# Optimization experiments

Hardware: AMD Instinct MI355X
Metric: run time of the kernel (lower is better)

## Reference

```python
import jax, jax.numpy as jnp
import numpy as np

LEAKY_SLOPE = 0.2
DENSITY = 0.05


def setup_inputs() -> dict:
    key = jax.random.key(0)
    k1, k2, k3, k4, k5, k6 = jax.random.split(key, 6)
    N, F_in, F_out = 8192, 128, 64
    h = jax.random.normal(k1, (N, F_in), dtype=jnp.float32)
    # Linear(in, out, bias=False) weight is [out, in]
    W = jax.random.normal(k2, (F_out, F_in), dtype=jnp.float32) * (1.0 / np.sqrt(F_in))
    a_left = jax.random.normal(k3, (F_out,), dtype=jnp.float32) * 0.1
    a_right = jax.random.normal(k4, (F_out,), dtype=jnp.float32) * 0.1
    vals = jax.random.uniform(k5, (N, N), dtype=jnp.float32)
    keep = jax.random.uniform(k6, (N, N)) < DENSITY
    adj = jnp.where(keep, vals, 0.0)  # raw adjacency; self-loops added in reference
    return {"h": h, "W": W, "a_left": a_left, "a_right": a_right, "adj": adj}


def reference(h, W, a_left, a_right, adj):
    N = adj.shape[0]
    A = adj + jnp.eye(N, dtype=adj.dtype)          # A = adjacency + I (self-loops)
    mask = jnp.abs(A) > 0                          # valued-mask support
    Wh = h @ W.T                                   # [N, F_out]
    e_left = Wh @ a_left                           # [N]
    e_right = Wh @ a_right                         # [N]
    e = e_left[:, None] + e_right[None, :]         # [N, N] additive scores
    e = jnp.where(e >= 0, e, LEAKY_SLOPE * e)      # LeakyReLU(0.2)
    e = jnp.where(mask, e, -jnp.inf)               # masked_fill(mask==0, -inf)
    attention = jax.nn.softmax(e, axis=1) * A      # valued masking post-softmax
    # dropout p=0.0 -> identity (eval-mode reference)
    return attention @ Wh                          # [N, F_out]
```

## Files before the change

kernel.cpp:

```cpp
#include <hip/hip_runtime.h>
#include <hip/hip_bf16.h>
#include <hip/hip_fp16.h>

#define N    8192
#define FIN  128
#define FOUT 64
#define LEAKY 0.2f
#define CAPQ 256
#define LOG2E 1.44269504088896340736f

struct alignas(8) Ent { unsigned joff; float w; };

__global__ __launch_bounds__(256) void wh_eLR_kernel(
    const float* __restrict__ h, const float* __restrict__ Wm,
    const float* __restrict__ aL, const float* __restrict__ aR,
    __half* __restrict__ Whh, float* __restrict__ eL2, float* __restrict__ eR2)
{
    __shared__ float sW[FOUT][FIN + 1];
    __shared__ float sh[4][FIN];
    const int t = threadIdx.x;
    const int rbase = blockIdx.x * 4;

    for (int idx = t; idx < FOUT * FIN; idx += 256)
        sW[idx >> 7][idx & 127] = Wm[idx];
    for (int idx = t; idx < 4 * FIN; idx += 256)
        sh[idx >> 7][idx & 127] = h[(size_t)(rbase + (idx >> 7)) * FIN + (idx & 127)];
    __syncthreads();

    const int wv = t >> 6, f = t & 63;
    const int row = rbase + wv;
    float acc = 0.f;
    #pragma unroll 16
    for (int k = 0; k < FIN; ++k) acc += sh[wv][k] * sW[f][k];
    Whh[(size_t)row * FOUT + f] = __float2half_rn(acc);

    float vl = acc * aL[f];
    float vr = acc * aR[f];
    #pragma unroll
    for (int d = 32; d > 0; d >>= 1) {
        vl += __shfl_down(vl, d, 64);
        vr += __shfl_down(vr, d, 64);
    }
    if (f == 0) { eL2[row] = vl * LOG2E; eR2[row] = vr * LOG2E; }
}

__global__ __launch_bounds__(256) void gat_row_kernel(
    const float* __restrict__ adj, const __half* __restrict__ Whh,
    const float* __restrict__ eL2p, const float* __restrict__ eR2p,
    float* __restrict__ out)
{
    __shared__ Ent ent[4][CAPQ];
    __shared__ float4 facc[4][16];
    __shared__ float fpsum[4];

    const int t = threadIdx.x;
    const int wv = t >> 6;
    const int lane = t & 63;
    const int row = blockIdx.x;

    const float el = eL2p[row];
    const float4* __restrict__ arow4 = (const float4*)(adj + (size_t)row * N);
    const char* __restrict__ er2b = (const char*)eR2p;
    const char* __restrict__ whb  = (const char*)Whh;
    Ent* __restrict__ myent = ent[wv];

    const unsigned l7 = ((unsigned)((wv << 11) + lane * 4)) << 7;
    const unsigned l7u[4] = {l7, l7 + 128, l7 + 256, l7 + 384};
    const unsigned row7 = ((unsigned)row) << 7;
    const int rcl = (row >> 8) - (wv << 3);

    int base = 0;

    #pragma unroll
    for (int c = 0; c < 8; ++c) {
        const float4 a4 = arow4[(wv << 9) + c * 64 + lane];
        const float av[4] = {a4.x, a4.y, a4.z, a4.w};
        const unsigned cbits = ((unsigned)c) << 15;
        const bool cdiag = (c == rcl);
        #pragma unroll
        for (int u = 0; u < 4; ++u) {
            float a = av[u];
            if (cdiag) {
                if ((cbits + l7u[u]) == row7) a += 1.0f;
            }
            const bool nz = (a != 0.f);
            const unsigned long long m = __ballot(nz);
            const int before = __builtin_amdgcn_mbcnt_hi(
                (unsigned)(m >> 32),
                __builtin_amdgcn_mbcnt_lo((unsigned)m, 0));
            if (nz) {
                Ent e; e.joff = cbits + l7u[u]; e.w = a;
                myent[base + before] = e;
            }
            base += (int)__popcll(m);
        }
    }
    const int cnt = min(base, CAPQ - 16);
    if (lane < 16) { myent[cnt + lane].joff = 0; myent[cnt + lane].w = 0.f; }

    asm volatile("s_waitcnt lgkmcnt(0)" ::: "memory");

    float lsum = 0.f;
    for (int k = lane; k < cnt; k += 64) {
        const Ent e = myent[k];
        const float er = *(const float*)(er2b + (e.joff >> 5));
        float y = el + er;
        y = fmaxf(y, LEAKY * y);
        const float p = exp2f(y);
        myent[k].w = p * e.w;
        lsum += p;
    }
    #pragma unroll
    for (int d = 32; d > 0; d >>= 1) lsum += __shfl_down(lsum, d, 64);
    if (lane == 0) fpsum[wv] = lsum;

    asm volatile("s_waitcnt lgkmcnt(0)" ::: "memory");

    const int g = lane >> 4;
    const int fb = (lane & 15) * 8;
    const int cnt16 = (cnt + 15) & ~15;
    float ax = 0.f, ay = 0.f, az = 0.f, aw = 0.f;
    float bx = 0.f, by = 0.f, bz = 0.f, bw = 0.f;
    float cx = 0.f, cy = 0.f, cz = 0.f, cw = 0.f;
    float dx = 0.f, dy = 0.f, dz = 0.f, dw = 0.f;
    for (int k = g; k < cnt16; k += 16) {
        const Ent e0 = myent[k];
        const Ent e1 = myent[k + 4];
        const Ent e2 = myent[k + 8];
        const Ent e3 = myent[k + 12];
        const uint2 u0 = *(const uint2*)(whb + (e0.joff + fb));
        const uint2 u1 = *(const uint2*)(whb + (e1.joff + fb));
        const uint2 u2 = *(const uint2*)(whb + (e2.joff + fb));
        const uint2 u3 = *(const uint2*)(whb + (e3.joff + fb));
        const float2 f00 = __half22float2(*(const __half2*)&u0.x);
        const float2 f01 = __half22float2(*(const __half2*)&u0.y);
        const float2 f10 = __half22float2(*(const __half2*)&u1.x);
        const float2 f11 = __half22float2(*(const __half2*)&u1.y);
        const float2 f20 = __half22float2(*(const __half2*)&u2.x);
        const float2 f21 = __half22float2(*(const __half2*)&u2.y);
        const float2 f30 = __half22float2(*(const __half2*)&u3.x);
        const float2 f31 = __half22float2(*(const __half2*)&u3.y);
        ax += e0.w * f00.x; ay += e0.w * f00.y; az += e0.w * f01.x; aw += e0.w * f01.y;
        bx += e1.w * f10.x; by += e1.w * f10.y; bz += e1.w * f11.x; bw += e1.w * f11.y;
        cx += e2.w * f20.x; cy += e2.w * f20.y; cz += e2.w * f21.x; cw += e2.w * f21.y;
        dx += e3.w * f30.x; dy += e3.w * f30.y; dz += e3.w * f31.x; dw += e3.w * f31.y;
    }
    ax += bx; ay += by; az += bz; aw += bw;
    cx += dx; cy += dy; cz += dz; cw += dw;
    ax += cx; ay += cy; az += cz; aw += cw;
    #pragma unroll
    for (int d = 32; d >= 16; d >>= 1) {
        ax += __shfl_down(ax, d, 64);
        ay += __shfl_down(ay, d, 64);
        az += __shfl_down(az, d, 64);
        aw += __shfl_down(aw, d, 64);
    }
    if (lane < 16) {
        float4 p; p.x = ax; p.y = ay; p.z = az; p.w = aw;
        facc[wv][lane] = p;
    }
    __syncthreads();

    if (t < 16) {
        const float Z = fpsum[0] + fpsum[1] + fpsum[2] + fpsum[3];
        const float rz = 1.0f / Z;
        const float4 p0 = facc[0][t];
        const float4 p1 = facc[1][t];
        const float4 p2 = facc[2][t];
        const float4 p3 = facc[3][t];
        float4 r;
        r.x = (p0.x + p1.x + p2.x + p3.x) * rz;
        r.y = (p0.y + p1.y + p2.y + p3.y) * rz;
        r.z = (p0.z + p1.z + p2.z + p3.z) * rz;
        r.w = (p0.w + p1.w + p2.w + p3.w) * rz;
        *(float4*)(out + (size_t)row * FOUT + t * 4) = r;
    }
}

extern "C" void kernel_launch(void* const* d_in, const int* in_sizes, int n_in,
                              void* d_out, int out_size, void* d_ws, size_t ws_size,
                              hipStream_t stream) {
    const float* h   = (const float*)d_in[0];
    const float* Wm  = (const float*)d_in[1];
    const float* aL  = (const float*)d_in[2];
    const float* aR  = (const float*)d_in[3];
    const float* adj = (const float*)d_in[4];
    float* outp = (float*)d_out;

    __half* Whh = (__half*)d_ws;
    float* eL2  = (float*)((char*)d_ws + (size_t)N * FOUT * 2);
    float* eR2  = eL2 + N;

    wh_eLR_kernel<<<N / 4, 256, 0, stream>>>(h, Wm, aL, aR, Whh, eL2, eR2);
    gat_row_kernel<<<N, 256, 0, stream>>>(adj, Whh, eL2, eR2, outp);
}
```

Measured before the change: 81.79 us.

## Fuse softmax exponent pass into aggregation loop and batch adjacency row loads

The separate LDS pass that computed exp2 scores and rewrote entry weights is removed. The exp and LeakyReLU are now computed inline in the gather/accumulate loop, and the softmax denominator is accumulated alongside. The adjacency row is loaded as two batches of four float4 loads to expose more memory-level parallelism. An occupancy hint of 8 blocks is added to the launch bounds. In exchange, each lane in a 16-lane group recomputes the same exponentials redundantly and may have higher register pressure.

```diff
diff --git a/kernel.cpp b/kernel.cpp
--- a/kernel.cpp
+++ b/kernel.cpp
@@ -44,7 +44,7 @@
     if (f == 0) { eL2[row] = vl * LOG2E; eR2[row] = vr * LOG2E; }
 }
 
-__global__ __launch_bounds__(256) void gat_row_kernel(
+__global__ __launch_bounds__(256, 8) void gat_row_kernel(
     const float* __restrict__ adj, const __half* __restrict__ Whh,
     const float* __restrict__ eL2p, const float* __restrict__ eR2p,
     float* __restrict__ out)
@@ -68,51 +68,43 @@
     const unsigned l7u[4] = {l7, l7 + 128, l7 + 256, l7 + 384};
     const unsigned row7 = ((unsigned)row) << 7;
     const int rcl = (row >> 8) - (wv << 3);
+    const int qb = (wv << 9) + lane;
 
     int base = 0;
 
     #pragma unroll
-    for (int c = 0; c < 8; ++c) {
-        const float4 a4 = arow4[(wv << 9) + c * 64 + lane];
-        const float av[4] = {a4.x, a4.y, a4.z, a4.w};
-        const unsigned cbits = ((unsigned)c) << 15;
-        const bool cdiag = (c == rcl);
+    for (int half = 0; half < 2; ++half) {
+        float4 b[4];
         #pragma unroll
-        for (int u = 0; u < 4; ++u) {
-            float a = av[u];
-            if (cdiag) {
-                if ((cbits + l7u[u]) == row7) a += 1.0f;
+        for (int c = 0; c < 4; ++c)
+            b[c] = arow4[qb + (half * 4 + c) * 64];
+        #pragma unroll
+        for (int c = 0; c < 4; ++c) {
+            const int cg = half * 4 + c;
+            const float av[4] = {b[c].x, b[c].y, b[c].z, b[c].w};
+            const unsigned cbits = ((unsigned)cg) << 15;
+            const bool cdiag = (cg == rcl);
+            #pragma unroll
+            for (int u = 0; u < 4; ++u) {
+                float a = av[u];
+                if (cdiag) {
+                    if ((cbits + l7u[u]) == row7) a += 1.0f;
+                }
+                const bool nz = (a != 0.f);
+                const unsigned long long m = __ballot(nz);
+                const int before = __builtin_amdgcn_mbcnt_hi(
+                    (unsigned)(m >> 32),
+                    __builtin_amdgcn_mbcnt_lo((unsigned)m, 0));
+                if (nz) {
+                    Ent e; e.joff = cbits + l7u[u]; e.w = a;
+                    myent[base + before] = e;
+                }
+                base += (int)__popcll(m);
             }
-            const bool nz = (a != 0.f);
-            const unsigned long long m = __ballot(nz);
-            const int before = __builtin_amdgcn_mbcnt_hi(
-                (unsigned)(m >> 32),
-                __builtin_amdgcn_mbcnt_lo((unsigned)m, 0));
-            if (nz) {
-                Ent e; e.joff = cbits + l7u[u]; e.w = a;
-                myent[base + before] = e;
-            }
-            base += (int)__popcll(m);
         }
     }
     const int cnt = min(base, CAPQ - 16);
-    if (lane < 16) { myent[cnt + lane].joff = 0; myent[cnt + lane].w = 0.f; }
-
-    asm volatile("s_waitcnt lgkmcnt(0)" ::: "memory");
-
-    float lsum = 0.f;
-    for (int k = lane; k < cnt; k += 64) {
-        const Ent e = myent[k];
-        const float er = *(const float*)(er2b + (e.joff >> 5));
-        float y = el + er;
-        y = fmaxf(y, LEAKY * y);
-        const float p = exp2f(y);
-        myent[k].w = p * e.w;
-        lsum += p;
-    }
-    #pragma unroll
-    for (int d = 32; d > 0; d >>= 1) lsum += __shfl_down(lsum, d, 64);
-    if (lane == 0) fpsum[wv] = lsum;
+    if (lane < 16) { Ent z; z.joff = 0; z.w = 0.f; myent[cnt + lane] = z; }
 
     asm volatile("s_waitcnt lgkmcnt(0)" ::: "memory");
 
@@ -123,15 +115,30 @@
     float bx = 0.f, by = 0.f, bz = 0.f, bw = 0.f;
     float cx = 0.f, cy = 0.f, cz = 0.f, cw = 0.f;
     float dx = 0.f, dy = 0.f, dz = 0.f, dw = 0.f;
+    float psum = 0.f;
     for (int k = g; k < cnt16; k += 16) {
         const Ent e0 = myent[k];
         const Ent e1 = myent[k + 4];
         const Ent e2 = myent[k + 8];
         const Ent e3 = myent[k + 12];
+        const float er0 = *(const float*)(er2b + (e0.joff >> 5));
+        const float er1 = *(const float*)(er2b + (e1.joff >> 5));
+        const float er2 = *(const float*)(er2b + (e2.joff >> 5));
+        const float er3 = *(const float*)(er2b + (e3.joff >> 5));
         const uint2 u0 = *(const uint2*)(whb + (e0.joff + fb));
         const uint2 u1 = *(const uint2*)(whb + (e1.joff + fb));
         const uint2 u2 = *(const uint2*)(whb + (e2.joff + fb));
         const uint2 u3 = *(const uint2*)(whb + (e3.joff + fb));
+        float y0 = el + er0; y0 = fmaxf(y0, LEAKY * y0);
+        float y1 = el + er1; y1 = fmaxf(y1, LEAKY * y1);
+        float y2 = el + er2; y2 = fmaxf(y2, LEAKY * y2);
+        float y3 = el + er3; y3 = fmaxf(y3, LEAKY * y3);
+        const float p0 = exp2f(y0), p1 = exp2f(y1);
+        const float p2 = exp2f(y2), p3 = exp2f(y3);
+        psum += (e0.w != 0.f ? p0 : 0.f) + (e1.w != 0.f ? p1 : 0.f)
+              + (e2.w != 0.f ? p2 : 0.f) + (e3.w != 0.f ? p3 : 0.f);
+        const float w0 = p0 * e0.w, w1 = p1 * e1.w;
+        const float w2 = p2 * e2.w, w3 = p3 * e3.w;
         const float2 f00 = __half22float2(*(const __half2*)&u0.x);
         const float2 f01 = __half22float2(*(const __half2*)&u0.y);
         const float2 f10 = __half22float2(*(const __half2*)&u1.x);
@@ -140,10 +147,10 @@
         const float2 f21 = __half22float2(*(const __half2*)&u2.y);
         const float2 f30 = __half22float2(*(const __half2*)&u3.x);
         const float2 f31 = __half22float2(*(const __half2*)&u3.y);
-        ax += e0.w * f00.x; ay += e0.w * f00.y; az += e0.w * f01.x; aw += e0.w * f01.y;
-        bx += e1.w * f10.x; by += e1.w * f10.y; bz += e1.w * f11.x; bw += e1.w * f11.y;
-        cx += e2.w * f20.x; cy += e2.w * f20.y; cz += e2.w * f21.x; cw += e2.w * f21.y;
-        dx += e3.w * f30.x; dy += e3.w * f30.y; dz += e3.w * f31.x; dw += e3.w * f31.y;
+        ax += w0 * f00.x; ay += w0 * f00.y; az += w0 * f01.x; aw += w0 * f01.y;
+        bx += w1 * f10.x; by += w1 * f10.y; bz += w1 * f11.x; bw += w1 * f11.y;
+        cx += w2 * f20.x; cy += w2 * f20.y; cz += w2 * f21.x; cw += w2 * f21.y;
+        dx += w3 * f30.x; dy += w3 * f30.y; dz += w3 * f31.x; dw += w3 * f31.y;
     }
     ax += bx; ay += by; az += bz; aw += bw;
     cx += dx; cy += dy; cz += dz; cw += dw;
@@ -154,11 +161,10 @@
         ay += __shfl_down(ay, d, 64);
         az += __shfl_down(az, d, 64);
         aw += __shfl_down(aw, d, 64);
-    }
-    if (lane < 16) {
-        float4 p; p.x = ax; p.y = ay; p.z = az; p.w = aw;
-        facc[wv][lane] = p;
-    }
+        psum += __shfl_down(psum, d, 64);
+    }
+    if (lane < 16) { float4 p; p.x = ax; p.y = ay; p.z = az; p.w = aw; facc[wv][lane] = p; }
+    if (lane == 0) fpsum[wv] = psum;
     __syncthreads();
 
     if (t < 16) {
```

After: 77.02 us. -5.8%, faster.
